# Kernel tuning notes

Hardware: AMD Instinct MI355X
Metric: run time of the kernel (lower is better)

Reference implementation:

```python
import jax, jax.numpy as jnp
import numpy as np


def setup_inputs() -> dict:
    key = jax.random.key(0)
    ks = jax.random.split(key, 6)
    B, N, D, C = 16, 4096, 1024, 4
    bags = jax.random.normal(ks[0], (B, N, D), dtype=jnp.float32)
    query = jax.random.normal(ks[1], (D,), dtype=jnp.float32)
    W1 = jax.random.normal(ks[2], (3 * D, 512), dtype=jnp.float32) * 0.02
    b1 = jax.random.normal(ks[3], (512,), dtype=jnp.float32) * 0.02
    W2 = jax.random.normal(ks[4], (512, C), dtype=jnp.float32) * 0.02
    b2 = jax.random.normal(ks[5], (C,), dtype=jnp.float32) * 0.02
    return {"bags": bags, "query": query, "W1": W1, "b1": b1, "W2": W2, "b2": b2}


def reference(bags, query, W1, b1, W2, b2):
    # bags: [B, N, D] instance features (frozen feat_extractor output)
    mean_pool = jnp.mean(bags, axis=1)                     # [B, D]
    max_pool = jnp.max(bags, axis=1)                       # [B, D]
    # attention pooling: softmax over instances of <bag_i, query>
    scores = jax.nn.softmax(jnp.einsum('bnd,d->bn', bags, query), axis=1)  # [B, N]
    attn_pool = jnp.einsum('bn,bnd->bd', scores, bags)     # [B, D]
    x = jnp.concatenate([mean_pool, max_pool, attn_pool], axis=-1)  # [B, 3D]
    x = x @ W1 + b1
    x = x @ W2 + b2
    return x
```

## Files before the change

### kernel.cpp

```cpp
#include <hip/hip_runtime.h>
#include <math.h>

#define BNUM 16
#define NNUM 4096
#define DNUM 1024
#define CNUM 4
#define HNUM 512

#define SCH   32
#define ROWS  (NNUM / SCH)
#define RPW   (ROWS / 4)

#define NMAIN (SCH * BNUM)
#define NWEFFBLK 768
#define GRID1 (NMAIN + NWEFFBLK + 1)

#define PSTRIDE 3080
#define XOFF    ((size_t)NMAIN * PSTRIDE)
#define WOFF    (XOFF + 16)
#define BIASOFF (WOFF + (size_t)3 * DNUM * 4)

#define NEG_INF (-__builtin_inff())

typedef float vf4 __attribute__((ext_vector_type(4)));

__global__ __launch_bounds__(256) void k_stage1(const float* __restrict__ bags,
                                                const float* __restrict__ query,
                                                const float* __restrict__ W1,
                                                const float* __restrict__ b1,
                                                const float* __restrict__ W2,
                                                const float* __restrict__ b2,
                                                float* __restrict__ ws) {
    const int tid  = threadIdx.x;
    const int wave = tid >> 6;
    const int lane = tid & 63;

    if (blockIdx.x >= NMAIN) {
        const vf4* w2 = (const vf4*)W2;
        const int wb = blockIdx.x - NMAIN;
        if (wb < NWEFFBLK) {
            const int k = wb * 4 + wave;
            const float* r = W1 + (size_t)k * HNUM;
            float a0 = 0.f, a1 = 0.f, a2 = 0.f, a3 = 0.f;
#pragma unroll
            for (int t = 0; t < 8; ++t) {
                const int j = lane * 8 + t;
                const float wv = r[j];
                const vf4   w  = w2[j];
                a0 += wv * w.x; a1 += wv * w.y; a2 += wv * w.z; a3 += wv * w.w;
            }
#pragma unroll
            for (int off = 32; off; off >>= 1) {
                a0 += __shfl_xor(a0, off, 64);
                a1 += __shfl_xor(a1, off, 64);
                a2 += __shfl_xor(a2, off, 64);
                a3 += __shfl_xor(a3, off, 64);
            }
            if (lane == 0) {
                vf4 rv; rv.x = a0; rv.y = a1; rv.z = a2; rv.w = a3;
                ((vf4*)(ws + WOFF))[k] = rv;
            }
        } else if (wave == 0) {
            float a0 = 0.f, a1 = 0.f, a2 = 0.f, a3 = 0.f;
#pragma unroll
            for (int t = 0; t < 8; ++t) {
                const int j = lane * 8 + t;
                const float bv = b1[j];
                const vf4   w  = w2[j];
                a0 += bv * w.x; a1 += bv * w.y; a2 += bv * w.z; a3 += bv * w.w;
            }
#pragma unroll
            for (int off = 32; off; off >>= 1) {
                a0 += __shfl_xor(a0, off, 64);
                a1 += __shfl_xor(a1, off, 64);
                a2 += __shfl_xor(a2, off, 64);
                a3 += __shfl_xor(a3, off, 64);
            }
            if (lane == 0) {
                float* bias = ws + BIASOFF;
                bias[0] = a0 + b2[0]; bias[1] = a1 + b2[1];
                bias[2] = a2 + b2[2]; bias[3] = a3 + b2[3];
            }
        }
        return;
    }

    const int chunk = blockIdx.x & (SCH - 1);
    const int b     = blockIdx.x >> 5;

    const vf4* q4 = (const vf4*)query;
    vf4 q[4];
#pragma unroll
    for (int s = 0; s < 4; ++s) q[s] = q4[s * 64 + lane];

    vf4 sum[4], mx[4], acc[4];
#pragma unroll
    for (int s = 0; s < 4; ++s) {
        sum[s] = (vf4)0.f;
        acc[s] = (vf4)0.f;
        mx[s]  = (vf4)NEG_INF;
    }
    float m = NEG_INF, l = 0.f;

    const int n0 = chunk * ROWS + wave * RPW;
    const vf4* base = (const vf4*)(bags + (size_t)b * NNUM * DNUM);

    for (int r = 0; r < RPW; r += 2) {
        const vf4* rowA = base + (size_t)(n0 + r) * (DNUM / 4);
        const vf4* rowB = rowA + (DNUM / 4);
        vf4 va[4], vb[4];
#pragma unroll
        for (int s = 0; s < 4; ++s) va[s] = rowA[s * 64 + lane];
#pragma unroll
        for (int s = 0; s < 4; ++s) vb[s] = rowB[s * 64 + lane];

        float pa = 0.f, pb = 0.f;
#pragma unroll
        for (int s = 0; s < 4; ++s) {
            pa += va[s].x * q[s].x + va[s].y * q[s].y + va[s].z * q[s].z + va[s].w * q[s].w;
            pb += vb[s].x * q[s].x + vb[s].y * q[s].y + vb[s].z * q[s].z + vb[s].w * q[s].w;
        }
#pragma unroll
        for (int off = 32; off; off >>= 1) {
            pa += __shfl_xor(pa, off, 64);
            pb += __shfl_xor(pb, off, 64);
        }

        const float mnew = fmaxf(m, fmaxf(pa, pb));
        if (mnew > m) {
            const float alpha = __expf(m - mnew);
            l *= alpha;
#pragma unroll
            for (int s = 0; s < 4; ++s) acc[s] *= alpha;
            m = mnew;
        }
        const float wa = __expf(pa - m);
        const float wb = __expf(pb - m);
        l += wa + wb;

#pragma unroll
        for (int s = 0; s < 4; ++s) {
            sum[s] += va[s] + vb[s];
            mx[s].x = fmaxf(mx[s].x, fmaxf(va[s].x, vb[s].x));
            mx[s].y = fmaxf(mx[s].y, fmaxf(va[s].y, vb[s].y));
            mx[s].z = fmaxf(mx[s].z, fmaxf(va[s].z, vb[s].z));
            mx[s].w = fmaxf(mx[s].w, fmaxf(va[s].w, vb[s].w));
            acc[s] += wa * va[s] + wb * vb[s];
        }
    }

    __shared__ float buf[4][DNUM];
    __shared__ float sm[4], sl[4];
    if (lane == 0) { sm[wave] = m; sl[wave] = l; }

    float* wsp = ws + (size_t)(b * SCH + chunk) * PSTRIDE;

#pragma unroll
    for (int s = 0; s < 4; ++s) ((vf4*)(&buf[wave][s * 256]))[lane] = sum[s];
    __syncthreads();
    {
        vf4 a0 = ((vf4*)buf[0])[tid];
        vf4 a1 = ((vf4*)buf[1])[tid];
        vf4 a2 = ((vf4*)buf[2])[tid];
        vf4 a3 = ((vf4*)buf[3])[tid];
        ((vf4*)wsp)[tid] = a0 + a1 + a2 + a3;
    }
    __syncthreads();

#pragma unroll
    for (int s = 0; s < 4; ++s) ((vf4*)(&buf[wave][s * 256]))[lane] = mx[s];
    __syncthreads();
    {
        vf4 a0 = ((vf4*)buf[0])[tid];
        vf4 a1 = ((vf4*)buf[1])[tid];
        vf4 a2 = ((vf4*)buf[2])[tid];
        vf4 a3 = ((vf4*)buf[3])[tid];
        vf4 r;
        r.x = fmaxf(fmaxf(a0.x, a1.x), fmaxf(a2.x, a3.x));
        r.y = fmaxf(fmaxf(a0.y, a1.y), fmaxf(a2.y, a3.y));
        r.z = fmaxf(fmaxf(a0.z, a1.z), fmaxf(a2.z, a3.z));
        r.w = fmaxf(fmaxf(a0.w, a1.w), fmaxf(a2.w, a3.w));
        ((vf4*)(wsp + 1024))[tid] = r;
    }
    __syncthreads();

#pragma unroll
    for (int s = 0; s < 4; ++s) ((vf4*)(&buf[wave][s * 256]))[lane] = acc[s];
    __syncthreads();
    {
        const float m0 = sm[0], m1 = sm[1], m2 = sm[2], m3 = sm[3];
        const float mb = fmaxf(fmaxf(m0, m1), fmaxf(m2, m3));
        const float e0 = __expf(m0 - mb), e1 = __expf(m1 - mb);
        const float e2 = __expf(m2 - mb), e3 = __expf(m3 - mb);
        vf4 a0 = ((vf4*)buf[0])[tid];
        vf4 a1 = ((vf4*)buf[1])[tid];
        vf4 a2 = ((vf4*)buf[2])[tid];
        vf4 a3 = ((vf4*)buf[3])[tid];
        ((vf4*)(wsp + 2048))[tid] = a0 * e0 + a1 * e1 + a2 * e2 + a3 * e3;
        if (tid == 0) {
            wsp[3072] = mb;
            wsp[3073] = sl[0] * e0 + sl[1] * e1 + sl[2] * e2 + sl[3] * e3;
        }
    }
}

__global__ __launch_bounds__(256) void k_finish(const float* __restrict__ ws,
                                                float* __restrict__ out) {
    const int b    = blockIdx.x;
    const int dg   = blockIdx.y;
    const int tid  = threadIdx.x;
    const int wave = tid >> 6, lane = tid & 63;
    const int d    = dg * 256 + tid;

    __shared__ float eS[SCH];
    __shared__ float lbS;
    __shared__ float red[4][4];

    const float* pbag = ws + (size_t)b * SCH * PSTRIDE;

    if (wave == 0) {
        const float* p = pbag + (size_t)(lane & (SCH - 1)) * PSTRIDE;
        const float mlane = (lane < SCH) ? p[3072] : NEG_INF;
        const float llane = (lane < SCH) ? p[3073] : 0.f;
        float mb = mlane;
#pragma unroll
        for (int off = 32; off; off >>= 1) mb = fmaxf(mb, __shfl_xor(mb, off, 64));
        const float e = __expf(mlane - mb);
        float lb = llane * e;
#pragma unroll
        for (int off = 32; off; off >>= 1) lb += __shfl_xor(lb, off, 64);
        if (lane < SCH) eS[lane] = e;
        if (lane == 0) lbS = lb;
    }
    __syncthreads();
    const float inv_lb = 1.f / lbS;

    float fs = 0.f, fa = 0.f, fm = NEG_INF;
    for (int c = 0; c < SCH; ++c) {
        const float* p = pbag + (size_t)c * PSTRIDE;
        fs += p[d];
        fm = fmaxf(fm, p[1024 + d]);
        fa += eS[c] * p[2048 + d];
    }
    const float xm = fs * (1.f / NNUM);
    const float xa = fa * inv_lb;

    const vf4* weff = (const vf4*)(ws + WOFF);
    const vf4 w0 = weff[d];
    const vf4 w1 = weff[DNUM + d];
    const vf4 w2 = weff[2 * DNUM + d];
    float c0 = xm * w0.x + fm * w1.x + xa * w2.x;
    float c1 = xm * w0.y + fm * w1.y + xa * w2.y;
    float c2 = xm * w0.z + fm * w1.z + xa * w2.z;
    float c3 = xm * w0.w + fm * w1.w + xa * w2.w;
#pragma unroll
    for (int off = 32; off; off >>= 1) {
        c0 += __shfl_xor(c0, off, 64);
        c1 += __shfl_xor(c1, off, 64);
        c2 += __shfl_xor(c2, off, 64);
        c3 += __shfl_xor(c3, off, 64);
    }
    if (lane == 0) { red[wave][0] = c0; red[wave][1] = c1; red[wave][2] = c2; red[wave][3] = c3; }
    __syncthreads();
    if (tid < 4) {
        float v = red[0][tid] + red[1][tid] + red[2][tid] + red[3][tid];
        if (dg == 0) v += (ws + BIASOFF)[tid];
        atomicAdd(&out[b * 4 + tid], v);
    }
}

extern "C" void kernel_launch(void* const* d_in, const int* in_sizes, int n_in,
                              void* d_out, int out_size, void* d_ws, size_t ws_size,
                              hipStream_t stream) {
    const float* bags  = (const float*)d_in[0];
    const float* query = (const float*)d_in[1];
    const float* W1    = (const float*)d_in[2];
    const float* b1    = (const float*)d_in[3];
    const float* W2    = (const float*)d_in[4];
    const float* b2    = (const float*)d_in[5];
    float* out = (float*)d_out;
    float* ws  = (float*)d_ws;

    hipMemsetAsync(out, 0, (size_t)out_size * sizeof(float), stream);
    k_stage1<<<GRID1,            256, 0, stream>>>(bags, query, W1, b1, W2, b2, ws);
    k_finish<<<dim3(BNUM, 4),    256, 0, stream>>>(ws, out);
}
```

Before: 378.5 us.

## Fold output zeroing into stage1, use nontemporal bag loads, widen finish grid

Removes the separate memset launch by having the extra last block of stage1 zero the 64 output floats. Bag rows are loaded with nontemporal hints, since they are streamed once and should not pollute cache. The finish kernel now splits the 32 chunk partials across the four waves and combines them through shared memory, with 16 column groups per bag instead of 4, giving more parallel blocks. The cost is extra atomics per bag and a shared-memory reduction step.

```diff
diff --git a/kernel.cpp b/kernel.cpp
--- a/kernel.cpp
+++ b/kernel.cpp
@@ -30,7 +30,8 @@
                                                 const float* __restrict__ b1,
                                                 const float* __restrict__ W2,
                                                 const float* __restrict__ b2,
-                                                float* __restrict__ ws) {
+                                                float* __restrict__ ws,
+                                                float* __restrict__ out) {
     const int tid  = threadIdx.x;
     const int wave = tid >> 6;
     const int lane = tid & 63;
@@ -81,6 +82,8 @@
                 bias[0] = a0 + b2[0]; bias[1] = a1 + b2[1];
                 bias[2] = a2 + b2[2]; bias[3] = a3 + b2[3];
             }
+        } else if (wave == 1) {
+            out[lane] = 0.f;
         }
         return;
     }
@@ -110,9 +113,9 @@
         const vf4* rowB = rowA + (DNUM / 4);
         vf4 va[4], vb[4];
 #pragma unroll
-        for (int s = 0; s < 4; ++s) va[s] = rowA[s * 64 + lane];
-#pragma unroll
-        for (int s = 0; s < 4; ++s) vb[s] = rowB[s * 64 + lane];
+        for (int s = 0; s < 4; ++s) va[s] = __builtin_nontemporal_load(&rowA[s * 64 + lane]);
+#pragma unroll
+        for (int s = 0; s < 4; ++s) vb[s] = __builtin_nontemporal_load(&rowB[s * 64 + lane]);
 
         float pa = 0.f, pb = 0.f;
 #pragma unroll
@@ -210,11 +213,11 @@
     const int dg   = blockIdx.y;
     const int tid  = threadIdx.x;
     const int wave = tid >> 6, lane = tid & 63;
-    const int d    = dg * 256 + tid;
+    const int d    = dg * 64 + lane;
 
     __shared__ float eS[SCH];
     __shared__ float lbS;
-    __shared__ float red[4][4];
+    __shared__ float sred[3][4][64];
 
     const float* pbag = ws + (size_t)b * SCH * PSTRIDE;
 
@@ -233,39 +236,55 @@
         if (lane == 0) lbS = lb;
     }
     __syncthreads();
-    const float inv_lb = 1.f / lbS;
 
     float fs = 0.f, fa = 0.f, fm = NEG_INF;
-    for (int c = 0; c < SCH; ++c) {
+#pragma unroll
+    for (int i = 0; i < 8; ++i) {
+        const int c = wave * 8 + i;
         const float* p = pbag + (size_t)c * PSTRIDE;
         fs += p[d];
         fm = fmaxf(fm, p[1024 + d]);
         fa += eS[c] * p[2048 + d];
     }
-    const float xm = fs * (1.f / NNUM);
-    const float xa = fa * inv_lb;
-
-    const vf4* weff = (const vf4*)(ws + WOFF);
-    const vf4 w0 = weff[d];
-    const vf4 w1 = weff[DNUM + d];
-    const vf4 w2 = weff[2 * DNUM + d];
-    float c0 = xm * w0.x + fm * w1.x + xa * w2.x;
-    float c1 = xm * w0.y + fm * w1.y + xa * w2.y;
-    float c2 = xm * w0.z + fm * w1.z + xa * w2.z;
-    float c3 = xm * w0.w + fm * w1.w + xa * w2.w;
-#pragma unroll
-    for (int off = 32; off; off >>= 1) {
-        c0 += __shfl_xor(c0, off, 64);
-        c1 += __shfl_xor(c1, off, 64);
-        c2 += __shfl_xor(c2, off, 64);
-        c3 += __shfl_xor(c3, off, 64);
-    }
-    if (lane == 0) { red[wave][0] = c0; red[wave][1] = c1; red[wave][2] = c2; red[wave][3] = c3; }
-    __syncthreads();
-    if (tid < 4) {
-        float v = red[0][tid] + red[1][tid] + red[2][tid] + red[3][tid];
-        if (dg == 0) v += (ws + BIASOFF)[tid];
-        atomicAdd(&out[b * 4 + tid], v);
+    sred[0][wave][lane] = fs;
+    sred[1][wave][lane] = fm;
+    sred[2][wave][lane] = fa;
+    __syncthreads();
+
+    if (wave == 0) {
+        fs = sred[0][0][lane] + sred[0][1][lane] + sred[0][2][lane] + sred[0][3][lane];
+        fm = fmaxf(fmaxf(sred[1][0][lane], sred[1][1][lane]),
+                   fmaxf(sred[1][2][lane], sred[1][3][lane]));
+        fa = sred[2][0][lane] + sred[2][1][lane] + sred[2][2][lane] + sred[2][3][lane];
+
+        const float xm = fs * (1.f / NNUM);
+        const float xa = fa / lbS;
+
+        const vf4* weff = (const vf4*)(ws + WOFF);
+        const vf4 w0 = weff[d];
+        const vf4 w1 = weff[DNUM + d];
+        const vf4 w2 = weff[2 * DNUM + d];
+        float c0 = xm * w0.x + fm * w1.x + xa * w2.x;
+        float c1 = xm * w0.y + fm * w1.y + xa * w2.y;
+        float c2 = xm * w0.z + fm * w1.z + xa * w2.z;
+        float c3 = xm * w0.w + fm * w1.w + xa * w2.w;
+#pragma unroll
+        for (int off = 32; off; off >>= 1) {
+            c0 += __shfl_xor(c0, off, 64);
+            c1 += __shfl_xor(c1, off, 64);
+            c2 += __shfl_xor(c2, off, 64);
+            c3 += __shfl_xor(c3, off, 64);
+        }
+        if (lane == 0) {
+            if (dg == 0) {
+                const float* bias = ws + BIASOFF;
+                c0 += bias[0]; c1 += bias[1]; c2 += bias[2]; c3 += bias[3];
+            }
+            atomicAdd(&out[b * 4 + 0], c0);
+            atomicAdd(&out[b * 4 + 1], c1);
+            atomicAdd(&out[b * 4 + 2], c2);
+            atomicAdd(&out[b * 4 + 3], c3);
+        }
     }
 }
 
@@ -281,7 +300,6 @@
     float* out = (float*)d_out;
     float* ws  = (float*)d_ws;
 
-    hipMemsetAsync(out, 0, (size_t)out_size * sizeof(float), stream);
-    k_stage1<<<GRID1,            256, 0, stream>>>(bags, query, W1, b1, W2, b2, ws);
-    k_finish<<<dim3(BNUM, 4),    256, 0, stream>>>(ws, out);
+    k_stage1<<<GRID1,          256, 0, stream>>>(bags, query, W1, b1, W2, b2, ws, out);
+    k_finish<<<dim3(BNUM, 16), 256, 0, stream>>>(ws, out);
 }
```

Measured after the change: 360.8 us. 1.05x faster.
